# Optimization experiments

Hardware: AMD Instinct MI355X
Metric: run time of the kernel (lower is better)

## Reference

```python
import jax, jax.numpy as jnp
from jax import lax
import numpy as np

# dims: batch, in_channels, out_channels, spatial, kernel, padding
B, IC, OC, H, W, K, PAD = 4, 64, 64, 32, 32, 3, 1


def setup_inputs() -> dict:
    key = jax.random.key(0)
    k1, k2, k3, k4 = jax.random.split(key, 4)
    # x is a binary (+/-1) activation in this stochastic binary network
    x = jnp.sign(jax.random.normal(k1, (B, IC, H, W), jnp.float32))
    x = jnp.where(x == 0, 1.0, x)
    # q: small per-unit correction probabilities
    q = jax.random.uniform(k2, (B, IC, H, W), jnp.float32) * 1e-3
    # xavier_uniform with sigmoid gain (=1.0), as in _reset_parameters
    fan_in, fan_out = IC * K * K, OC * K * K
    bound = float(np.sqrt(6.0 / (fan_in + fan_out)))
    weight = jax.random.uniform(k3, (OC, IC, K, K), jnp.float32, -bound, bound)
    bbound = float(1.0 / np.sqrt(fan_in))
    bias = jax.random.uniform(k4, (OC,), jnp.float32, -bbound, bbound)
    return {"x": x, "q": q, "weight": weight, "bias": bias}


def _forward(x, q, weight, bias, key):
    pad = 2 * (K // 2) - PAD  # = 1 for k=3, padding=1
    # a0 = conv(x), NCHW / OIHW
    a0 = lax.conv_general_dilated(x, weight, (1, 1), [(PAD, PAD), (PAD, PAD)]) \
         + bias[None, :, None, None]                      # [B,OC,H,W]
    p0 = jax.nn.sigmoid(a0)
    # stochastic binary sample new_x in {-1,+1}; sample is non-differentiable
    new_x = 2.0 * jax.random.bernoulli(key, p0).astype(p0.dtype) - 1.0

    Kf = jnp.flip(weight, (2, 3))                         # flipped kernel
    a0_ = jnp.pad(a0, ((0, 0), (0, 0), (pad, pad), (pad, pad)))     # [B,OC,H+K-1,W+K-1]
    p0_ = jnp.pad(p0, ((0, 0), (0, 0), (pad, pad), (pad, pad)))
    y_ = jnp.pad(new_x, ((0, 0), (0, 0), (pad, pad), (pad, pad)))

    # Fused version of _compute_conv_diffs + _compute_delta_sum: instead of
    # materializing the full [K,K,B,OC,IC,H,W] tensor, process each (l1,l2)
    # shift (K*K = 9 static iterations), same math.
    delta_q = jnp.zeros((B, OC, H + K - 1, W + K - 1), p0.dtype)
    for l1 in range(K):
        for l2 in range(K):
            # a[l1,l2] : pre-activation if input bit (l1,l2) were flipped
            a_l = a0_[:, :, None, l1:l1 + H, l2:l2 + W] \
                  - 2.0 * x[:, None] * Kf[None, :, :, l1, l2, None, None]  # [B,OC,IC,H,W]
            p_l = jax.nn.sigmoid(a_l)
            add = jnp.sum((p_l - p0_[:, :, None, l1:l1 + H, l2:l2 + W]) * q[:, None],
                          axis=2) * (-y_[:, :, l1:l1 + H, l2:l2 + W])       # [B,OC,H,W]
            delta_q = delta_q.at[:, :, l1:l1 + H, l2:l2 + W].add(add)
    delta_q = delta_q[:, :, pad:-pad, pad:-pad]           # [B,OC,H,W]

    # delta_0: zero in value, carries gradient of p0 (straight-through trick)
    delta_0 = -new_x * (p0 - lax.stop_gradient(p0))
    qs = jnp.sum(q, axis=(1, 2, 3), keepdims=True)        # [B,1,1,1]
    new_q = delta_0 * (1.0 - qs) + delta_q
    # stride == 1 -> the [::stride] slicing is a no-op
    return new_x, new_q


def reference(x, q, weight, bias):
    return _forward(x, q, weight, bias, jax.random.key(42))
```

## Files before the change

### kernel.cpp

```cpp
#include <hip/hip_runtime.h>
#include <cstdint>


typedef __attribute__((ext_vector_type(4))) int   i32x4;
typedef __attribute__((ext_vector_type(8))) short s16x8;
typedef __attribute__((ext_vector_type(4))) float f32x4;

static constexpr int OFF_X8   = 0;
static constexpr int OFF_XQH  = 295936;
static constexpr int OFF_QH   = 887808;
static constexpr int OFF_WD   = 1479680;
static constexpr int OFF_WB   = 1627136;
static constexpr int OFF_W2B  = 1700864;

__device__ __forceinline__ uint32_t rotl32(uint32_t v, int n) {
  return (v << n) | (v >> (32 - n));
}

__device__ __forceinline__ unsigned short f2bf(float f) {
  uint32_t u = __float_as_uint(f);
  uint32_t r = (u + 0x7FFFu + ((u >> 16) & 1u)) >> 16;
  return (unsigned short)r;
}

__device__ __forceinline__ float threefry_u(uint32_t j) {
  uint32_t x0 = 0u, x1 = j;
  const uint32_t ks1 = 42u, ks2 = 0x1BD11BDAu ^ 42u;
  x0 += 0u; x1 += ks1;
#define QR(rot) { x0 += x1; x1 = rotl32(x1, rot); x1 ^= x0; }
  QR(13) QR(15) QR(26) QR(6)
  x0 += ks1; x1 += ks2 + 1u;
  QR(17) QR(29) QR(16) QR(24)
  x0 += ks2; x1 += 0u + 2u;
  QR(13) QR(15) QR(26) QR(6)
  x0 += 0u; x1 += ks1 + 3u;
  QR(17) QR(29) QR(16) QR(24)
  x0 += ks1; x1 += ks2 + 4u;
  QR(13) QR(15) QR(26) QR(6)
  x0 += ks2; x1 += 0u + 5u;
#undef QR
  uint32_t bits = x0 ^ x1;
  return __uint_as_float((bits >> 9) | 0x3F800000u) - 1.0f;
}

__global__ __launch_bounds__(256) void prep_kernel(
    const float* __restrict__ x, const float* __restrict__ q,
    const float* __restrict__ weight, char* __restrict__ ws) {
  const int blk = blockIdx.x;
  const int tid = threadIdx.x;

  if (blk < 128) {
    const int b = blk >> 5;
    const int h = blk & 31;
    __shared__ char           x8s[2048];
    __shared__ unsigned short xqs[2048];
    __shared__ unsigned short qs [2048];
    const int ic = tid >> 2;
    const int w0 = (tid & 3) * 8;
    const int src = ((b * 64 + ic) * 32 + h) * 32 + w0;
    float4 xa = *(const float4*)(x + src);
    float4 xb = *(const float4*)(x + src + 4);
    float4 qa = *(const float4*)(q + src);
    float4 qb = *(const float4*)(q + src + 4);
    float xv[8] = {xa.x, xa.y, xa.z, xa.w, xb.x, xb.y, xb.z, xb.w};
    float qv[8] = {qa.x, qa.y, qa.z, qa.w, qb.x, qb.y, qb.z, qb.w};
#pragma unroll
    for (int j = 0; j < 8; ++j) {
      int a = (w0 + j) * 64 + ic;
      x8s[a] = (char)(int)xv[j];
      xqs[a] = f2bf(xv[j] * qv[j]);
      qs[a]  = f2bf(qv[j]);
    }
    __syncthreads();
    const int rowel = ((b * 34 + h + 1) * 34 + 1) * 64;
    ((uint2*)(ws + OFF_X8 + rowel))[tid]      = ((const uint2*)x8s)[tid];
    ((uint4*)(ws + OFF_XQH + rowel * 2))[tid] = ((const uint4*)xqs)[tid];
    ((uint4*)(ws + OFF_QH  + rowel * 2))[tid] = ((const uint4*)qs)[tid];
  } else if (blk < 132) {
    const int b = blk - 128;
    for (int k = tid; k < 8448; k += 256) {
      int cell = k >> 6;
      int ic = k & 63;
      int hp, wp;
      if (cell < 34)       { hp = 0;          wp = cell; }
      else if (cell < 68)  { hp = 33;         wp = cell - 34; }
      else if (cell < 100) { hp = cell - 67;  wp = 0; }
      else                 { hp = cell - 99;  wp = 33; }
      int a = ((b * 34 + hp) * 34 + wp) * 64 + ic;
      ((char*)(ws + OFF_X8))[a] = 0;
      ((unsigned short*)(ws + OFF_XQH))[a] = 0;
      ((unsigned short*)(ws + OFF_QH))[a]  = 0;
    }
  } else {
    int k  = (blk - 132) * 256 + tid;
    int ic = k & 63;
    int t  = k >> 6;
    int oc  = t & 63;
    int tap = t >> 6;
    int kh = tap / 3, kw = tap % 3;
    float Wv = weight[((oc * 64 + ic) * 3 + kh) * 3 + kw];
    long long wi = llrint((double)Wv * 2147483648.0);
    char* wd = ws + OFF_WD;
#pragma unroll
    for (int dig = 0; dig < 4; ++dig) {
      signed char d = (signed char)(wi & 0xFF);
      wd[dig * 36864 + k] = d;
      wi = (wi - (long long)d) >> 8;
    }
    ((unsigned short*)(ws + OFF_WB))[k]  = f2bf(Wv);
    ((unsigned short*)(ws + OFF_W2B))[k] = f2bf(Wv * Wv);
  }
}

__global__ __launch_bounds__(256) void main_kernel(
    const char* __restrict__ ws, const float* __restrict__ bias,
    float* __restrict__ out) {
  const char* x8            = ws + OFF_X8;
  const unsigned short* xqh = (const unsigned short*)(ws + OFF_XQH);
  const unsigned short* qh  = (const unsigned short*)(ws + OFF_QH);
  const char* wd            = ws + OFF_WD;
  const unsigned short* wb  = (const unsigned short*)(ws + OFF_WB);
  const unsigned short* w2b = (const unsigned short*)(ws + OFF_W2B);

  const int b  = blockIdx.x >> 6;
  const int h  = (blockIdx.x >> 1) & 31;
  const int nt = blockIdx.x & 1;

  const int octile = threadIdx.x >> 6;
  const int lane   = threadIdx.x & 63;
  const int quad   = lane >> 4;
  const int l16    = lane & 15;

  i32x4 accI[4];
#pragma unroll
  for (int d = 0; d < 4; ++d) accI[d] = (i32x4){0, 0, 0, 0};
  f32x4 aC1 = {0.f, 0.f, 0.f, 0.f};
  f32x4 aC2 = {0.f, 0.f, 0.f, 0.f};

  const int aoff_i8 = (octile * 16 + l16) * 64 + quad * 16;
  const int aoff_bf = (octile * 16 + l16) * 64 + quad * 8;

#pragma unroll
  for (int kh = 0; kh < 3; ++kh) {
#pragma unroll
    for (int kw = 0; kw < 3; ++kw) {
      const int tap = kh * 3 + kw;
      i32x4 aI[4];
#pragma unroll
      for (int d = 0; d < 4; ++d)
        aI[d] = *(const i32x4*)(wd + d * 36864 + tap * 4096 + aoff_i8);
      s16x8 aW0 = *(const s16x8*)(wb  + tap * 4096 + aoff_bf);
      s16x8 aW1 = *(const s16x8*)(wb  + tap * 4096 + aoff_bf + 32);
      s16x8 aV0 = *(const s16x8*)(w2b + tap * 4096 + aoff_bf);
      s16x8 aV1 = *(const s16x8*)(w2b + tap * 4096 + aoff_bf + 32);
      const int pix = ((b * 34 + h + kh) * 34 + (nt * 16 + l16 + kw)) * 64;
      i32x4 bI  = *(const i32x4*)(x8 + pix + quad * 16);
      s16x8 bX0 = *(const s16x8*)(xqh + pix + quad * 8);
      s16x8 bX1 = *(const s16x8*)(xqh + pix + 32 + quad * 8);
      s16x8 bQ0 = *(const s16x8*)(qh  + pix + quad * 8);
      s16x8 bQ1 = *(const s16x8*)(qh  + pix + 32 + quad * 8);
#pragma unroll
      for (int d = 0; d < 4; ++d)
        accI[d] = __builtin_amdgcn_mfma_i32_16x16x64_i8(aI[d], bI, accI[d], 0, 0, 0);
      aC1 = __builtin_amdgcn_mfma_f32_16x16x32_bf16(aW0, bX0, aC1, 0, 0, 0);
      aC1 = __builtin_amdgcn_mfma_f32_16x16x32_bf16(aW1, bX1, aC1, 0, 0, 0);
      aC2 = __builtin_amdgcn_mfma_f32_16x16x32_bf16(aV0, bQ0, aC2, 0, 0, 0);
      aC2 = __builtin_amdgcn_mfma_f32_16x16x32_bf16(aV1, bQ1, aC2, 0, 0, 0);
    }
  }

  const int w = nt * 16 + l16;
#pragma unroll
  for (int r = 0; r < 4; ++r) {
    const int ocr = octile * 16 + quad * 4 + r;
    double a0 = (((double)accI[3][r] * 256.0 + (double)accI[2][r]) * 256.0 +
                 (double)accI[1][r]) * 256.0 + (double)accI[0][r];
    a0 = a0 * (1.0 / 2147483648.0) + (double)bias[ocr];
    double p0d = 1.0 / (1.0 + exp(-a0));
    const int o = ((b * 64 + ocr) * 32 + h) * 32 + w;
    float su = threefry_u((uint32_t)o);
    float nx = ((double)su < p0d) ? 1.0f : -1.0f;
    float p0 = (float)p0d;
    float s1 = p0 * (1.0f - p0);
    float s2 = s1 * (1.0f - 2.0f * p0);
    float dq = 2.0f * nx * (s1 * aC1[r] - s2 * aC2[r]);
    out[o] = nx;
    out[262144 + o] = dq;
  }
}

extern "C" void kernel_launch(void* const* d_in, const int* in_sizes, int n_in,
                              void* d_out, int out_size, void* d_ws, size_t ws_size,
                              hipStream_t stream) {
  const float* x      = (const float*)d_in[0];
  const float* q      = (const float*)d_in[1];
  const float* weight = (const float*)d_in[2];
  const float* bias   = (const float*)d_in[3];
  float* out = (float*)d_out;
  char* ws   = (char*)d_ws;

  prep_kernel<<<276, 256, 0, stream>>>(x, q, weight, ws);
  main_kernel<<<256, 256, 0, stream>>>(ws, bias, out);
}
```

Baseline: 75.31 us.

## Split conv taps across two wave halves with LDS reduction in main kernel

Doubles the main kernel block to 512 threads. The 9 kernel taps are split 5/4 between two halves of the block, and the partial MFMA accumulators are exchanged through shared memory. Each half then finishes two of the four output rows in the epilogue (sigmoid, threefry, store). The aim is to cut the serial per-wave MFMA chain and spread the expensive double-precision epilogue across more waves, since only 256 blocks run. The cost is an LDS round trip, a block barrier and an uneven 5/4 tap split.

```diff
diff --git a/kernel.cpp b/kernel.cpp
--- a/kernel.cpp
+++ b/kernel.cpp
@@ -112,7 +112,7 @@
   }
 }
 
-__global__ __launch_bounds__(256) void main_kernel(
+__global__ __launch_bounds__(512) void main_kernel(
     const char* __restrict__ ws, const float* __restrict__ bias,
     float* __restrict__ out) {
   const char* x8            = ws + OFF_X8;
@@ -122,12 +122,16 @@
   const unsigned short* wb  = (const unsigned short*)(ws + OFF_WB);
   const unsigned short* w2b = (const unsigned short*)(ws + OFF_W2B);
 
+  __shared__ int lds[4 * 2 * 12 * 64];
+
   const int b  = blockIdx.x >> 6;
   const int h  = (blockIdx.x >> 1) & 31;
   const int nt = blockIdx.x & 1;
 
-  const int octile = threadIdx.x >> 6;
-  const int lane   = threadIdx.x & 63;
+  const int tid    = threadIdx.x;
+  const int octile = (tid >> 6) & 3;
+  const int half   = tid >> 8;
+  const int lane   = tid & 63;
   const int quad   = lane >> 4;
   const int l16    = lane & 15;
 
@@ -140,11 +144,14 @@
   const int aoff_i8 = (octile * 16 + l16) * 64 + quad * 16;
   const int aoff_bf = (octile * 16 + l16) * 64 + quad * 8;
 
-#pragma unroll
-  for (int kh = 0; kh < 3; ++kh) {
-#pragma unroll
-    for (int kw = 0; kw < 3; ++kw) {
-      const int tap = kh * 3 + kw;
+  const int tbase = half ? 5 : 0;
+  const int tnum  = half ? 4 : 5;
+#pragma unroll
+  for (int i = 0; i < 5; ++i) {
+    if (i < tnum) {
+      const int tap = tbase + i;
+      const int kh = tap / 3;
+      const int kw = tap - kh * 3;
       i32x4 aI[4];
 #pragma unroll
       for (int d = 0; d < 4; ++d)
@@ -169,9 +176,38 @@
     }
   }
 
+  {
+    const int rp = 2 * (1 - half);
+    int* wr = lds + ((octile * 2 + half) * 12) * 64 + lane;
+#pragma unroll
+    for (int d = 0; d < 4; ++d) {
+      wr[(d) * 64]     = accI[d][rp];
+      wr[(4 + d) * 64] = accI[d][rp + 1];
+    }
+    wr[8 * 64]  = __float_as_int(aC1[rp]);
+    wr[9 * 64]  = __float_as_int(aC1[rp + 1]);
+    wr[10 * 64] = __float_as_int(aC2[rp]);
+    wr[11 * 64] = __float_as_int(aC2[rp + 1]);
+  }
+  __syncthreads();
+  const int r0 = 2 * half;
+  {
+    const int* rd = lds + ((octile * 2 + (1 - half)) * 12) * 64 + lane;
+#pragma unroll
+    for (int d = 0; d < 4; ++d) {
+      accI[d][r0]     += rd[(d) * 64];
+      accI[d][r0 + 1] += rd[(4 + d) * 64];
+    }
+    aC1[r0]     += __int_as_float(rd[8 * 64]);
+    aC1[r0 + 1] += __int_as_float(rd[9 * 64]);
+    aC2[r0]     += __int_as_float(rd[10 * 64]);
+    aC2[r0 + 1] += __int_as_float(rd[11 * 64]);
+  }
+
   const int w = nt * 16 + l16;
 #pragma unroll
-  for (int r = 0; r < 4; ++r) {
+  for (int rr = 0; rr < 2; ++rr) {
+    const int r = r0 + rr;
     const int ocr = octile * 16 + quad * 4 + r;
     double a0 = (((double)accI[3][r] * 256.0 + (double)accI[2][r]) * 256.0 +
                  (double)accI[1][r]) * 256.0 + (double)accI[0][r];
@@ -200,5 +236,5 @@
   char* ws   = (char*)d_ws;
 
   prep_kernel<<<276, 256, 0, stream>>>(x, q, weight, ws);
-  main_kernel<<<256, 256, 0, stream>>>(ws, bias, out);
-}
+  main_kernel<<<256, 512, 0, stream>>>(ws, bias, out);
+}
```

Result: slower. 79.07 us (+5.0%).
